# Performance work log

Hardware: AMD Instinct MI355X
Metric: run time of the kernel (lower is better)

## Reference

```python
import jax, jax.numpy as jnp
import numpy as np

N_EMBD = 1024
N_HEAD = 16
HEAD_DIM = N_EMBD // N_HEAD
B, T = 2, 2048


def setup_inputs() -> dict:
    key = jax.random.key(0)
    ks = jax.random.split(key, 9)
    s = 1.0 / np.sqrt(N_EMBD)
    return {
        "x": jax.random.normal(ks[0], (B, T, N_EMBD), dtype=jnp.float32),
        "Wq": jax.random.normal(ks[1], (N_EMBD, N_EMBD), dtype=jnp.float32) * s,
        "bq": jax.random.normal(ks[2], (N_EMBD,), dtype=jnp.float32) * s,
        "Wk": jax.random.normal(ks[3], (N_EMBD, N_EMBD), dtype=jnp.float32) * s,
        "bk": jax.random.normal(ks[4], (N_EMBD,), dtype=jnp.float32) * s,
        "Wv": jax.random.normal(ks[5], (N_EMBD, N_EMBD), dtype=jnp.float32) * s,
        "bv": jax.random.normal(ks[6], (N_EMBD,), dtype=jnp.float32) * s,
        "Wp": jax.random.normal(ks[7], (N_EMBD, N_EMBD), dtype=jnp.float32) * s,
        "bp": jax.random.normal(ks[8], (N_EMBD,), dtype=jnp.float32) * s,
    }


def reference(x, Wq, bq, Wk, bk, Wv, bv, Wp, bp):
    b, t, c = x.shape
    # torch Linear: y = x @ W.T + b
    def proj(W, bias):
        y = jnp.einsum('btc,oc->bto', x, W) + bias
        return y.reshape(b, t, N_HEAD, HEAD_DIM).transpose(0, 2, 1, 3)  # [B,H,T,D]

    q = proj(Wq, bq)
    k = proj(Wk, bk)
    v = proj(Wv, bv)

    scale = 1.0 / np.sqrt(HEAD_DIM).astype(np.float32)
    scores = jnp.einsum('bhqd,bhkd->bhqk', q, k) * scale  # [B,H,T,T]
    causal = jnp.tril(jnp.ones((t, t), dtype=bool))
    scores = jnp.where(causal[None, None], scores, jnp.float32(-jnp.inf))
    attn = jax.nn.softmax(scores, axis=-1)
    out = jnp.einsum('bhqk,bhkd->bhqd', attn, v)  # [B,H,T,D]
    out = out.transpose(0, 2, 1, 3).reshape(b, t, c)
    out = jnp.einsum('btc,oc->bto', out, Wp) + bp
    return out
```

## Files before the change

### kernel.cpp

```cpp
#include <hip/hip_runtime.h>
#include <hip/hip_bf16.h>

#define TT 2048
#define MM 4096
#define KS_LD 72

typedef __attribute__((ext_vector_type(8))) short bf16x8;
typedef __attribute__((ext_vector_type(4))) float f32x4;

__device__ inline short f2bf(float f){
  union { float f; unsigned u; } x; x.f = f;
  unsigned r = x.u + 0x7FFFu + ((x.u >> 16) & 1u);
  return (short)(r >> 16);
}
__device__ inline int pk2bf(float a, float b){
  __hip_bfloat162 h2 = __float22bfloat162_rn(make_float2(a, b));
  return *(int*)&h2;
}

__device__ inline void async16(const void* g, void* l){
  __builtin_amdgcn_global_load_lds((const __attribute__((address_space(1))) void*)g,
                                   (__attribute__((address_space(3))) void*)l, 16, 0, 0);
}

__global__ void cvt_all(const float* __restrict__ x,
                        const float* __restrict__ Wq, const float* __restrict__ Wk,
                        const float* __restrict__ Wv, const float* __restrict__ Wp,
                        short* __restrict__ xb, short* __restrict__ Wqb, short* __restrict__ Wkb,
                        short* __restrict__ Wvb, short* __restrict__ Wpb){
  int b = blockIdx.x;
  const float* in; short* out; int base;
  if (b < 4096)      { in = x;  out = xb;  base = b; }
  else if (b < 5120) { in = Wq; out = Wqb; base = b - 4096; }
  else if (b < 6144) { in = Wk; out = Wkb; base = b - 5120; }
  else if (b < 7168) { in = Wv; out = Wvb; base = b - 6144; }
  else               { in = Wp; out = Wpb; base = b - 7168; }
  int i = base * 256 + threadIdx.x;
  float4 v = ((const float4*)in)[i];
  short4 o;
  o.x = f2bf(v.x); o.y = f2bf(v.y); o.z = f2bf(v.z); o.w = f2bf(v.w);
  ((short4*)out)[i] = o;
}

__device__ inline void gemm_core(const short* __restrict__ A, const short* __restrict__ Wm,
                                 short* As, short* Bs, int m0, int n0,
                                 int tid, int wm, int wn, int quad, int lr,
                                 f32x4 acc[4][4])
{
  const int prow = tid >> 2, pcol = (tid & 3) << 3;
  const short* Ap0 = A  + (size_t)(m0 + prow) * 1024 + pcol;
  const short* Ap1 = A  + (size_t)(m0 + prow + 64) * 1024 + pcol;
  const short* Bp0 = Wm + (size_t)(n0 + prow) * 1024 + pcol;
  const short* Bp1 = Wm + (size_t)(n0 + prow + 64) * 1024 + pcol;
  for (int kt = 0; kt < 16; ++kt){
    const int kk = kt * 64;
#pragma unroll
    for (int pn = 0; pn < 2; ++pn){
      async16(Ap0 + kk + pn*32, As + pn*4096 + (size_t)tid * 8);
      async16(Ap1 + kk + pn*32, As + pn*4096 + (size_t)(tid + 256) * 8);
      async16(Bp0 + kk + pn*32, Bs + pn*4096 + (size_t)tid * 8);
      async16(Bp1 + kk + pn*32, Bs + pn*4096 + (size_t)(tid + 256) * 8);
    }
    __syncthreads();
#pragma unroll
    for (int ks = 0; ks < 2; ++ks){
      bf16x8 aF[4], bF[4];
#pragma unroll
      for (int mt = 0; mt < 4; ++mt) aF[mt] = *(const bf16x8*)(As + ks*4096 + (wm*64 + mt*16 + lr)*32 + quad*8);
#pragma unroll
      for (int nt = 0; nt < 4; ++nt) bF[nt] = *(const bf16x8*)(Bs + ks*4096 + (wn*64 + nt*16 + lr)*32 + quad*8);
#pragma unroll
      for (int mt = 0; mt < 4; ++mt)
#pragma unroll
        for (int nt = 0; nt < 4; ++nt)
          acc[mt][nt] = __builtin_amdgcn_mfma_f32_16x16x32_bf16(aF[mt], bF[nt], acc[mt][nt], 0, 0, 0);
    }
    __syncthreads();
  }
}

__launch_bounds__(256, 3)
__global__ void gemm_qkv(const short* __restrict__ A,
                         const short* __restrict__ W0, const short* __restrict__ W1, const short* __restrict__ W2,
                         const float* __restrict__ b0, const float* __restrict__ b1, const float* __restrict__ b2,
                         short* __restrict__ Qo, short* __restrict__ Ko, short* __restrict__ Vt)
{
  __shared__ __align__(16) short smem[16384];
  short* As = smem;
  short* Bs = smem + 8192;
  const int z = blockIdx.z;
  const short* Wm   = (z == 0) ? W0 : ((z == 1) ? W1 : W2);
  const float* bias = (z == 0) ? b0 : ((z == 1) ? b1 : b2);
  const int tid = threadIdx.x;
  const int lane = tid & 63, wave = tid >> 6;
  const int wm = wave >> 1, wn = wave & 1;
  const int quad = lane >> 4, lr = lane & 15;
  const int m0 = blockIdx.y * 128, n0 = blockIdx.x * 128;

  f32x4 acc[4][4];
#pragma unroll
  for (int i = 0; i < 4; ++i)
#pragma unroll
    for (int j = 0; j < 4; ++j)
#pragma unroll
      for (int r = 0; r < 4; ++r) acc[i][j][r] = 0.f;

  gemm_core(A, Wm, As, Bs, m0, n0, tid, wm, wn, quad, lr, acc);

  const float qscale = 0.125f * 1.4426950408889634f;
  const int bB = m0 >> 11, t0 = m0 & 2047;

  if (z == 2){
#pragma unroll
    for (int nh = 0; nh < 2; ++nh){
      __syncthreads();
      if (wn == nh){
#pragma unroll
        for (int nt = 0; nt < 4; ++nt){
          int n = n0 + wn*64 + nt*16 + lr;
          float bv = bias[n];
          int n_l = nt*16 + lr;
#pragma unroll
          for (int mt = 0; mt < 4; ++mt)
#pragma unroll
            for (int r = 0; r < 4; ++r){
              int m_l = wm*64 + mt*16 + quad*4 + r;
              smem[n_l*136 + m_l] = f2bf(acc[mt][nt][r] + bv);
            }
        }
      }
      __syncthreads();
#pragma unroll
      for (int i = 0; i < 4; ++i){
        int c = tid + i*256;
        int rowN = c >> 4, ch = c & 15;
        int4 v = *(const int4*)(smem + rowN*136 + ch*8);
        int n = n0 + nh*64 + rowN;
        int hH = n >> 6, d = n & 63;
        *(int4*)(Vt + ((size_t)((bB<<4) + hH)*64 + d)*2048 + t0 + ch*8) = v;
      }
    }
    return;
  }

  short* dst = (z == 0) ? Qo : Ko;
#pragma unroll
  for (int nh = 0; nh < 2; ++nh){
    __syncthreads();
    if (wn == nh){
#pragma unroll
      for (int nt = 0; nt < 4; ++nt){
        int n_l = nt*16 + lr;
        float bv = bias[n0 + nh*64 + n_l];
#pragma unroll
        for (int mt = 0; mt < 4; ++mt){
#pragma unroll
          for (int r = 0; r < 4; ++r){
            int m_l = wm*64 + mt*16 + quad*4 + r;
            float v = acc[mt][nt][r] + bv;
            if (z == 0) v *= qscale;
            smem[m_l*72 + n_l] = f2bf(v);
          }
        }
      }
    }
    __syncthreads();
    const int hH = (n0 + nh*64) >> 6;
    short* dhead = dst + (size_t)((bB<<4) + hH) * 2048 * 64;
#pragma unroll
    for (int i = 0; i < 4; ++i){
      int c = tid + i*256;
      int rowm = c >> 3, ch = (c & 7) << 3;
      int4 v = *(const int4*)(smem + rowm*72 + ch);
      *(int4*)(dhead + (size_t)(t0 + rowm)*64 + ch) = v;
    }
  }
}

__launch_bounds__(256, 2)
__global__ void gemm_proj(const short* __restrict__ A, const short* __restrict__ Wm,
                          const float* __restrict__ bias, float* __restrict__ out)
{
  __shared__ __align__(16) short As[2*4096];
  __shared__ __align__(16) short Bs[2*2048];
  const int tid = threadIdx.x;
  const int lane = tid & 63, wave = tid >> 6;
  const int quad = lane >> 4, lr = lane & 15;
  const int m0 = blockIdx.y * 128, n0 = blockIdx.x * 64;

  const int prow = tid >> 2, pcol = (tid & 3) << 3;
  const short* Ap0 = A  + (size_t)(m0 + prow) * 1024 + pcol;
  const short* Ap1 = A  + (size_t)(m0 + prow + 64) * 1024 + pcol;
  const short* Bp0 = Wm + (size_t)(n0 + (tid >> 2)) * 1024 + pcol;

  f32x4 acc[2][4];
#pragma unroll
  for (int i = 0; i < 2; ++i)
#pragma unroll
    for (int j = 0; j < 4; ++j)
#pragma unroll
      for (int r = 0; r < 4; ++r) acc[i][j][r] = 0.f;

  for (int kt = 0; kt < 16; ++kt){
    const int kk = kt * 64;
#pragma unroll
    for (int pn = 0; pn < 2; ++pn){
      async16(Ap0 + kk + pn*32, As + pn*4096 + (size_t)tid * 8);
      async16(Ap1 + kk + pn*32, As + pn*4096 + (size_t)(tid + 256) * 8);
      async16(Bp0 + kk + pn*32, Bs + pn*2048 + (size_t)tid * 8);
    }
    __syncthreads();
#pragma unroll
    for (int ks = 0; ks < 2; ++ks){
      bf16x8 aF[2], bF[4];
#pragma unroll
      for (int mt = 0; mt < 2; ++mt) aF[mt] = *(const bf16x8*)(As + ks*4096 + (wave*32 + mt*16 + lr)*32 + quad*8);
#pragma unroll
      for (int nt = 0; nt < 4; ++nt) bF[nt] = *(const bf16x8*)(Bs + ks*2048 + (nt*16 + lr)*32 + quad*8);
#pragma unroll
      for (int mt = 0; mt < 2; ++mt)
#pragma unroll
        for (int nt = 0; nt < 4; ++nt)
          acc[mt][nt] = __builtin_amdgcn_mfma_f32_16x16x32_bf16(aF[mt], bF[nt], acc[mt][nt], 0, 0, 0);
    }
    __syncthreads();
  }

#pragma unroll
  for (int nt = 0; nt < 4; ++nt){
    int n = n0 + nt*16 + lr;
    float bv = bias[n];
#pragma unroll
    for (int mt = 0; mt < 2; ++mt){
      int mBase = m0 + wave*32 + mt*16 + quad*4;
#pragma unroll
      for (int r = 0; r < 4; ++r){
        int m = mBase + r;
        out[(size_t)m * 1024 + n] = acc[mt][nt][r] + bv;
      }
    }
  }
}

__launch_bounds__(256, 4)
__global__ void attn_kernel(const short* __restrict__ Q, const short* __restrict__ K,
                            const short* __restrict__ Vt, short* __restrict__ AO)
{
  __shared__ __align__(16) short Ks[64*KS_LD];
  __shared__ __align__(16) short Vs[64*KS_LD];
  __shared__ __align__(16) short Ps[4*16*KS_LD];
  const int tid = threadIdx.x, lane = tid & 63, wave = tid >> 6;
  const int quad = lane >> 4, lr = lane & 15;
  const int bid = blockIdx.x;
  const int chunk = bid >> 8;
  const int a = (bid >> 5) & 7;
  int qt;
  if      (chunk == 0) qt = 31 - a;
  else if (chunk == 1) qt = a;
  else if (chunk == 2) qt = 23 - a;
  else                 qt = 8 + a;
  const int hb = bid & 31;
  const int bidx = hb >> 4, h = hb & 15;
  const int q0 = qt * 64;
  const int wq = q0 + wave * 16;
  const short* Qh = Q  + (size_t)hb * TT * 64;
  const short* Kh = K  + (size_t)hb * TT * 64;
  const short* Vh = Vt + (size_t)hb * 64 * TT;
  short* Pw = Ps + wave * 16 * KS_LD;

  bf16x8 qf[2];
#pragma unroll
  for (int ks = 0; ks < 2; ++ks)
    qf[ks] = *(const bf16x8*)(Qh + (size_t)(wq + lr) * 64 + ks*32 + quad*8);

  f32x4 acc_o[4], l_acc;
#pragma unroll
  for (int r = 0; r < 4; ++r) l_acc[r] = 0.f;
#pragma unroll
  for (int dt = 0; dt < 4; ++dt)
#pragma unroll
    for (int r = 0; r < 4; ++r) acc_o[dt][r] = 0.f;

  const short one_bf = (short)0x3F80;
  const bf16x8 onesf = { one_bf, one_bf, one_bf, one_bf, one_bf, one_bf, one_bf, one_bf };

  const int srow = tid >> 3, scol = (tid & 7) << 3;

  const int nkv = qt + 1;
  for (int kv = 0; kv < nkv; ++kv){
    const int kv0 = kv * 64;
    __syncthreads();
#pragma unroll
    for (int s = 0; s < 2; ++s){
      *(int4*)(Ks + (srow + s*32) * KS_LD + scol) = *(const int4*)(Kh + (size_t)(kv0 + srow + s*32) * 64 + scol);
      *(int4*)(Vs + (srow + s*32) * KS_LD + scol) = *(const int4*)(Vh + (size_t)(srow + s*32) * TT + kv0 + scol);
    }
    __syncthreads();
    if (kv0 > wq + 15) continue;

    f32x4 s4[4];
#pragma unroll
    for (int nt = 0; nt < 4; ++nt)
#pragma unroll
      for (int r = 0; r < 4; ++r) s4[nt][r] = 0.f;
#pragma unroll
    for (int nt = 0; nt < 4; ++nt)
#pragma unroll
      for (int ks = 0; ks < 2; ++ks){
        bf16x8 kf = *(const bf16x8*)(Ks + (nt*16 + lr)*KS_LD + ks*32 + quad*8);
        s4[nt] = __builtin_amdgcn_mfma_f32_16x16x32_bf16(kf, qf[ks], s4[nt], 0, 0, 0);
      }

    const bool need_mask = (kv == nkv - 1);
    const int qglob = wq + lr;
#pragma unroll
    for (int nt = 0; nt < 4; ++nt){
      const int keyb = kv0 + nt*16 + quad*4;
      float pv[4];
#pragma unroll
      for (int r = 0; r < 4; ++r){
        float v = exp2f(s4[nt][r]);
        if (need_mask && keyb + r > qglob) v = 0.f;
        pv[r] = v;
      }
      int2 w;
      w.x = pk2bf(pv[0], pv[1]);
      w.y = pk2bf(pv[2], pv[3]);
      *(int2*)(Pw + lr*KS_LD + nt*16 + quad*4) = w;
    }

#pragma unroll
    for (int ks = 0; ks < 2; ++ks){
      bf16x8 ptf = *(const bf16x8*)(Pw + lr*KS_LD + ks*32 + quad*8);
      l_acc = __builtin_amdgcn_mfma_f32_16x16x32_bf16(onesf, ptf, l_acc, 0, 0, 0);
#pragma unroll
      for (int dt = 0; dt < 4; ++dt){
        bf16x8 vf = *(const bf16x8*)(Vs + (dt*16 + lr)*KS_LD + ks*32 + quad*8);
        acc_o[dt] = __builtin_amdgcn_mfma_f32_16x16x32_bf16(vf, ptf, acc_o[dt], 0, 0, 0);
      }
    }
  }

  const float inv = __builtin_amdgcn_rcpf(l_acc[0]);
#pragma unroll
  for (int dt = 0; dt < 4; ++dt){
    int2 w;
    w.x = pk2bf(acc_o[dt][0] * inv, acc_o[dt][1] * inv);
    w.y = pk2bf(acc_o[dt][2] * inv, acc_o[dt][3] * inv);
    *(int2*)(Pw + lr*KS_LD + dt*16 + quad*4) = w;
  }
#pragma unroll
  for (int i = 0; i < 2; ++i){
    int c = lane + i*64;
    int row = c >> 3, ch = c & 7;
    int4 v = *(const int4*)(Pw + row*KS_LD + ch*8);
    *(int4*)(AO + (size_t)(bidx*2048 + wq + row)*1024 + h*64 + ch*8) = v;
  }
}

extern "C" void kernel_launch(void* const* d_in, const int* in_sizes, int n_in,
                              void* d_out, int out_size, void* d_ws, size_t ws_size,
                              hipStream_t stream)
{
  const float* x  = (const float*)d_in[0];
  const float* Wq = (const float*)d_in[1];
  const float* bq = (const float*)d_in[2];
  const float* Wk = (const float*)d_in[3];
  const float* bk = (const float*)d_in[4];
  const float* Wv = (const float*)d_in[5];
  const float* bv = (const float*)d_in[6];
  const float* Wp = (const float*)d_in[7];
  const float* bp = (const float*)d_in[8];
  float* out = (float*)d_out;

  char* ws = (char*)d_ws;
  const size_t MB = 1024ull * 1024ull;
  short* Qb  = (short*)(ws + 0);
  short* Kb  = (short*)(ws + 8*MB);
  short* Vtb = (short*)(ws + 16*MB);
  short* AOb = (short*)(ws + 24*MB);
  short* xb  = (short*)(ws + 24*MB);
  short* Wqb = (short*)(ws + 32*MB);
  short* Wkb = (short*)(ws + 34*MB);
  short* Wvb = (short*)(ws + 36*MB);
  short* Wpb = (short*)(ws + 38*MB);

  cvt_all<<<8192, 256, 0, stream>>>(x, Wq, Wk, Wv, Wp, xb, Wqb, Wkb, Wvb, Wpb);
  gemm_qkv<<<dim3(8, 32, 3), 256, 0, stream>>>(xb, Wqb, Wkb, Wvb, bq, bk, bv, Qb, Kb, Vtb);
  attn_kernel<<<1024, 256, 0, stream>>>(Qb, Kb, Vtb, AOb);
  gemm_proj<<<dim3(16, 32), 256, 0, stream>>>(AOb, Wpb, bp, out);
}
```

Measured before the change: 186.6 us.

## Double-buffer K/V tiles with async global-to-LDS loads and XOR swizzle

```diff
diff --git a/kernel.cpp b/kernel.cpp
--- a/kernel.cpp
+++ b/kernel.cpp
@@ -3,7 +3,6 @@
 
 #define TT 2048
 #define MM 4096
-#define KS_LD 72
 
 typedef __attribute__((ext_vector_type(8))) short bf16x8;
 typedef __attribute__((ext_vector_type(4))) float f32x4;
@@ -246,9 +245,9 @@
 __global__ void attn_kernel(const short* __restrict__ Q, const short* __restrict__ K,
                             const short* __restrict__ Vt, short* __restrict__ AO)
 {
-  __shared__ __align__(16) short Ks[64*KS_LD];
-  __shared__ __align__(16) short Vs[64*KS_LD];
-  __shared__ __align__(16) short Ps[4*16*KS_LD];
+  __shared__ __align__(16) short Ks[2][4096];
+  __shared__ __align__(16) short Vs[2][4096];
+  __shared__ __align__(16) short Ps[4096];
   const int tid = threadIdx.x, lane = tid & 63, wave = tid >> 6;
   const int quad = lane >> 4, lr = lane & 15;
   const int bid = blockIdx.x;
@@ -266,13 +265,22 @@
   const short* Qh = Q  + (size_t)hb * TT * 64;
   const short* Kh = K  + (size_t)hb * TT * 64;
   const short* Vh = Vt + (size_t)hb * 64 * TT;
-  short* Pw = Ps + wave * 16 * KS_LD;
+  short* Pw = Ps + wave * 1024;
+
+  const int srow = tid >> 3;
+  const int ssw  = (tid & 7) ^ (srow & 7);
+  const short* Kp0 = Kh + (size_t)srow * 64 + ssw * 8;
+  const short* Vp0 = Vh + (size_t)srow * TT + ssw * 8;
 
   bf16x8 qf[2];
 #pragma unroll
   for (int ks = 0; ks < 2; ++ks)
     qf[ks] = *(const bf16x8*)(Qh + (size_t)(wq + lr) * 64 + ks*32 + quad*8);
 
+  const int lsw0 = (((0*4 + quad) ^ (lr & 7)) << 3);
+  const int lsw1 = (((1*4 + quad) ^ (lr & 7)) << 3);
+  const int qh2 = quad >> 1, qlo = (quad & 1) << 2;
+
   f32x4 acc_o[4], l_acc;
 #pragma unroll
   for (int r = 0; r < 4; ++r) l_acc[r] = 0.f;
@@ -284,61 +292,71 @@
   const short one_bf = (short)0x3F80;
   const bf16x8 onesf = { one_bf, one_bf, one_bf, one_bf, one_bf, one_bf, one_bf, one_bf };
 
-  const int srow = tid >> 3, scol = (tid & 7) << 3;
-
   const int nkv = qt + 1;
+  async16(Kp0,           &Ks[0][(size_t)tid * 8]);
+  async16(Kp0 + 32*64,   &Ks[0][(size_t)(tid + 256) * 8]);
+  async16(Vp0,           &Vs[0][(size_t)tid * 8]);
+  async16(Vp0 + 32*TT,   &Vs[0][(size_t)(tid + 256) * 8]);
+
+  int cur = 0;
   for (int kv = 0; kv < nkv; ++kv){
     const int kv0 = kv * 64;
     __syncthreads();
-#pragma unroll
-    for (int s = 0; s < 2; ++s){
-      *(int4*)(Ks + (srow + s*32) * KS_LD + scol) = *(const int4*)(Kh + (size_t)(kv0 + srow + s*32) * 64 + scol);
-      *(int4*)(Vs + (srow + s*32) * KS_LD + scol) = *(const int4*)(Vh + (size_t)(srow + s*32) * TT + kv0 + scol);
-    }
-    __syncthreads();
-    if (kv0 > wq + 15) continue;
-
-    f32x4 s4[4];
-#pragma unroll
-    for (int nt = 0; nt < 4; ++nt)
-#pragma unroll
-      for (int r = 0; r < 4; ++r) s4[nt][r] = 0.f;
-#pragma unroll
-    for (int nt = 0; nt < 4; ++nt)
+    if (kv + 1 < nkv){
+      const short* kp = Kp0 + (size_t)(kv + 1) * 4096;
+      const short* vp = Vp0 + (kv + 1) * 64;
+      const int nb = cur ^ 1;
+      async16(kp,          &Ks[nb][(size_t)tid * 8]);
+      async16(kp + 32*64,  &Ks[nb][(size_t)(tid + 256) * 8]);
+      async16(vp,          &Vs[nb][(size_t)tid * 8]);
+      async16(vp + 32*TT,  &Vs[nb][(size_t)(tid + 256) * 8]);
+    }
+    if (kv0 <= wq + 15){
+      f32x4 s4[4];
+#pragma unroll
+      for (int nt = 0; nt < 4; ++nt)
+#pragma unroll
+        for (int r = 0; r < 4; ++r) s4[nt][r] = 0.f;
+#pragma unroll
+      for (int nt = 0; nt < 4; ++nt){
+        bf16x8 kf0 = *(const bf16x8*)(&Ks[cur][(nt*16 + lr)*64 + lsw0]);
+        bf16x8 kf1 = *(const bf16x8*)(&Ks[cur][(nt*16 + lr)*64 + lsw1]);
+        s4[nt] = __builtin_amdgcn_mfma_f32_16x16x32_bf16(kf0, qf[0], s4[nt], 0, 0, 0);
+        s4[nt] = __builtin_amdgcn_mfma_f32_16x16x32_bf16(kf1, qf[1], s4[nt], 0, 0, 0);
+      }
+
+      const bool need_mask = (kv == nkv - 1);
+      const int qglob = wq + lr;
+#pragma unroll
+      for (int nt = 0; nt < 4; ++nt){
+        const int keyb = kv0 + nt*16 + quad*4;
+        float pv[4];
+#pragma unroll
+        for (int r = 0; r < 4; ++r){
+          float v = exp2f(s4[nt][r]);
+          if (need_mask && keyb + r > qglob) v = 0.f;
+          pv[r] = v;
+        }
+        int2 w;
+        w.x = pk2bf(pv[0], pv[1]);
+        w.y = pk2bf(pv[2], pv[3]);
+        const int g = nt*2 + qh2;
+        *(int2*)(Pw + lr*64 + ((g ^ (lr & 7)) << 3) + qlo) = w;
+      }
+
 #pragma unroll
       for (int ks = 0; ks < 2; ++ks){
-        bf16x8 kf = *(const bf16x8*)(Ks + (nt*16 + lr)*KS_LD + ks*32 + quad*8);
-        s4[nt] = __builtin_amdgcn_mfma_f32_16x16x32_bf16(kf, qf[ks], s4[nt], 0, 0, 0);
-      }
-
-    const bool need_mask = (kv == nkv - 1);
-    const int qglob = wq + lr;
-#pragma unroll
-    for (int nt = 0; nt < 4; ++nt){
-      const int keyb = kv0 + nt*16 + quad*4;
-      float pv[4];
-#pragma unroll
-      for (int r = 0; r < 4; ++r){
-        float v = exp2f(s4[nt][r]);
-        if (need_mask && keyb + r > qglob) v = 0.f;
-        pv[r] = v;
-      }
-      int2 w;
-      w.x = pk2bf(pv[0], pv[1]);
-      w.y = pk2bf(pv[2], pv[3]);
-      *(int2*)(Pw + lr*KS_LD + nt*16 + quad*4) = w;
-    }
-
-#pragma unroll
-    for (int ks = 0; ks < 2; ++ks){
-      bf16x8 ptf = *(const bf16x8*)(Pw + lr*KS_LD + ks*32 + quad*8);
-      l_acc = __builtin_amdgcn_mfma_f32_16x16x32_bf16(onesf, ptf, l_acc, 0, 0, 0);
-#pragma unroll
-      for (int dt = 0; dt < 4; ++dt){
-        bf16x8 vf = *(const bf16x8*)(Vs + (dt*16 + lr)*KS_LD + ks*32 + quad*8);
-        acc_o[dt] = __builtin_amdgcn_mfma_f32_16x16x32_bf16(vf, ptf, acc_o[dt], 0, 0, 0);
-      }
-    }
+        const int lsw = ks ? lsw1 : lsw0;
+        bf16x8 ptf = *(const bf16x8*)(Pw + lr*64 + lsw);
+        l_acc = __builtin_amdgcn_mfma_f32_16x16x32_bf16(onesf, ptf, l_acc, 0, 0, 0);
+#pragma unroll
+        for (int dt = 0; dt < 4; ++dt){
+          bf16x8 vf = *(const bf16x8*)(&Vs[cur][(dt*16 + lr)*64 + lsw]);
+          acc_o[dt] = __builtin_amdgcn_mfma_f32_16x16x32_bf16(vf, ptf, acc_o[dt], 0, 0, 0);
+        }
+      }
+    }
+    cur ^= 1;
   }
 
   const float inv = __builtin_amdgcn_rcpf(l_acc[0]);
@@ -347,13 +365,14 @@
     int2 w;
     w.x = pk2bf(acc_o[dt][0] * inv, acc_o[dt][1] * inv);
     w.y = pk2bf(acc_o[dt][2] * inv, acc_o[dt][3] * inv);
-    *(int2*)(Pw + lr*KS_LD + dt*16 + quad*4) = w;
+    const int g = dt*2 + qh2;
+    *(int2*)(Pw + lr*64 + ((g ^ (lr & 7)) << 3) + qlo) = w;
   }
 #pragma unroll
   for (int i = 0; i < 2; ++i){
     int c = lane + i*64;
     int row = c >> 3, ch = c & 7;
-    int4 v = *(const int4*)(Pw + row*KS_LD + ch*8);
+    int4 v = *(const int4*)(Pw + row*64 + ((ch ^ (row & 7)) << 3));
     *(int4*)(AO + (size_t)(bidx*2048 + wq + row)*1024 + h*64 + ch*8) = v;
   }
 }
```

Measured after the change: 180.5 us. 3.3% less time.
